# Kernel tuning notes

Measured on AMD Instinct MI355X. Metric: run time of the kernel, lower is better.

The kernel has to match this reference:

```python
import jax, jax.numpy as jnp
import numpy as np

N, C, D, E = 50000, 8, 64, 100000   # nodes, columns, dim, edges
L, H, FF, OUT = 2, 4, 64, 16        # layers, heads, dim_feedforward, out_channels
HD = D // H
EPS = 1e-5


def layer_norm(x, g, b):
    m = jnp.mean(x, axis=-1, keepdims=True)
    v = jnp.mean(jnp.square(x - m), axis=-1, keepdims=True)
    return (x - m) * jax.lax.rsqrt(v + EPS) * g + b


def encoder_layer(x, ipw, ipb, opw, opb, g1, b1, g2, b2, w1, bb1, w2, bb2):
    # x: [E, S, D]; post-norm TransformerEncoderLayer, relu, dropout=0 (eval)
    qkv = x @ ipw.T + ipb                      # [E, S, 3D]
    q, k, v = jnp.split(qkv, 3, axis=-1)
    Eb, S, _ = x.shape
    q = q.reshape(Eb, S, H, HD)
    k = k.reshape(Eb, S, H, HD)
    v = v.reshape(Eb, S, H, HD)
    scores = jnp.einsum('eqhd,ekhd->ehqk', q, k) / jnp.sqrt(jnp.asarray(HD, x.dtype))
    attn = jax.nn.softmax(scores, axis=-1)
    o = jnp.einsum('ehqk,ekhd->eqhd', attn, v).reshape(Eb, S, D)
    o = o @ opw.T + opb
    x = layer_norm(x + o, g1, b1)
    ff = jax.nn.relu(x @ w1.T + bb1) @ w2.T + bb2
    return layer_norm(x + ff, g2, b2)


def setup_inputs() -> dict:
    key = jax.random.key(0)
    ks = jax.random.split(key, 20)
    s = lambda *sh: 1.0 / np.sqrt(sh[-1])
    inp = {
        'x': jax.random.normal(ks[0], (N, C), jnp.float32),
        'edge_index': jax.random.randint(ks[1], (2, E), 0, N, jnp.int64),
        # NumEmbedder: per-column scalar -> D linear
        'num_w': jax.random.normal(ks[2], (C, D), jnp.float32) * 0.1,
        'num_b': jax.random.normal(ks[3], (C, D), jnp.float32) * 0.1,
        # per-layer TransformerGNN params (stacked over L)
        'bproj_w': jax.random.normal(ks[4], (L, D, D), jnp.float32) * s(D, D),
        'bproj_b': jnp.zeros((L, D), jnp.float32),
        'in_proj_w': jax.random.normal(ks[5], (L, 3 * D, D), jnp.float32) * s(D, D),
        'in_proj_b': jnp.zeros((L, 3 * D), jnp.float32),
        'out_proj_w': jax.random.normal(ks[6], (L, D, D), jnp.float32) * s(D, D),
        'out_proj_b': jnp.zeros((L, D), jnp.float32),
        'ln1_g': jnp.ones((L, D), jnp.float32), 'ln1_b': jnp.zeros((L, D), jnp.float32),
        'ln2_g': jnp.ones((L, D), jnp.float32), 'ln2_b': jnp.zeros((L, D), jnp.float32),
        'ff1_w': jax.random.normal(ks[7], (L, FF, D), jnp.float32) * s(FF, D),
        'ff1_b': jnp.zeros((L, FF), jnp.float32),
        'ff2_w': jax.random.normal(ks[8], (L, D, FF), jnp.float32) * s(D, FF),
        'ff2_b': jnp.zeros((L, D), jnp.float32),
        'out_w': jax.random.normal(ks[9], (OUT, D), jnp.float32) * s(OUT, D),
        'out_b': jnp.zeros((OUT,), jnp.float32),
    }
    return inp


def reference(x, edge_index, num_w, num_b, bproj_w, bproj_b, in_proj_w, in_proj_b,
              out_proj_w, out_proj_b, ln1_g, ln1_b, ln2_g, ln2_b,
              ff1_w, ff1_b, ff2_w, ff2_b, out_w, out_b):
    # column embedding: [N, C] -> [N, C, D] -> [N, C*D]
    h = (x[:, :, None] * num_w[None] + num_b[None]).reshape(N, C * D)
    src, tgt = edge_index[0], edge_index[1]
    cnt = jnp.clip(jax.ops.segment_sum(jnp.ones((E,), h.dtype), tgt, num_segments=N), 1.0)[:, None]
    for l in range(L):
        x_i = h[tgt].reshape(E, C, D)
        x_j = h[src].reshape(E, C, D) @ bproj_w[l].T + bproj_b[l]
        xc = jnp.concatenate([x_i, x_j], axis=1)              # [E, 2C, D]
        t = encoder_layer(xc, in_proj_w[l], in_proj_b[l], out_proj_w[l], out_proj_b[l],
                          ln1_g[l], ln1_b[l], ln2_g[l], ln2_b[l],
                          ff1_w[l], ff1_b[l], ff2_w[l], ff2_b[l])
        msg = t[:, :C, :].reshape(E, C * D)                   # slice target tokens
        h = jax.ops.segment_sum(msg, tgt, num_segments=N) / cnt  # mean aggr
    z = h.reshape(N, C, D) @ out_w.T + out_b                  # [N, C, OUT]
    z = jnp.sum(z, axis=1)
    return jax.nn.softmax(z, axis=1)
```

## Files before the change

### kernel.cpp

```cpp
#include <hip/hip_runtime.h>
#include <hip/hip_bf16.h>

#define NN 50000
#define EE 100000
#define LL 2

typedef __attribute__((ext_vector_type(8))) short short8;
typedef __attribute__((ext_vector_type(4))) float f32x4;

__device__ __forceinline__ short f2bf(float x) {
    __hip_bfloat16 b = __float2bfloat16(x);
    short s;
    __builtin_memcpy(&s, &b, 2);
    return s;
}
__device__ __forceinline__ unsigned us(short v) { return (unsigned)(unsigned short)v; }


__global__ __launch_bounds__(256)
void count_kernel(const int* __restrict__ tgt, int* __restrict__ cnt) {
    int e = blockIdx.x * 256 + threadIdx.x;
    if (e < EE) atomicAdd(&cnt[tgt[e]], 1);
}

__global__ __launch_bounds__(1024)
void scan_kernel(const int* __restrict__ cnt, int* __restrict__ off) {
    __shared__ int tmp[1024];
    __shared__ int carry;
    if (threadIdx.x == 0) carry = 0;
    __syncthreads();
    for (int base = 0; base < NN; base += 1024) {
        int i = base + threadIdx.x;
        int v = (i < NN) ? cnt[i] : 0;
        tmp[threadIdx.x] = v;
        __syncthreads();
        for (int d = 1; d < 1024; d <<= 1) {
            int t = (threadIdx.x >= d) ? tmp[threadIdx.x - d] : 0;
            __syncthreads();
            tmp[threadIdx.x] += t;
            __syncthreads();
        }
        int incl = tmp[threadIdx.x] + carry;
        if (i < NN) off[i + 1] = incl;
        __syncthreads();
        if (threadIdx.x == 1023) carry = incl;
        __syncthreads();
    }
    if (threadIdx.x == 0) off[0] = 0;
}

__global__ __launch_bounds__(256)
void fill_kernel(const int* __restrict__ tgt, const int* __restrict__ off,
                 int* __restrict__ fil, int* __restrict__ eidx) {
    int e = blockIdx.x * 256 + threadIdx.x;
    if (e < EE) {
        int t = tgt[e];
        int s = atomicAdd(&fil[t], 1);
        eidx[off[t] + s] = e;
    }
}

__global__ __launch_bounds__(256)
void recip_kernel(const int* __restrict__ cnt, float* __restrict__ rcnt) {
    int n = blockIdx.x * 256 + threadIdx.x;
    if (n < NN) rcnt[n] = 1.0f / fmaxf((float)cnt[n], 1.0f);
}

__global__ __launch_bounds__(256)
void embed_kernel(const float* __restrict__ x, const float* __restrict__ nw,
                  const float* __restrict__ nb, float* __restrict__ h0) {
    int gid = blockIdx.x * 256 + threadIdx.x;
    if (gid >= NN * 512) return;
    int n = gid >> 9, j = gid & 511;
    h0[gid] = x[n * 8 + (j >> 6)] * nw[j] + nb[j];
}

__global__ __launch_bounds__(256)
void prep_frags(const float* __restrict__ bpw, const float* __restrict__ ipw,
                const float* __restrict__ opw, const float* __restrict__ f1w,
                const float* __restrict__ f2w, short* __restrict__ wtb) {
    int gid = blockIdx.x * 256 + threadIdx.x;
    if (gid >= LL * 28672) return;
    int l = gid / 28672, u = gid % 28672;
    int f = u >> 9;
    int el = u & 511;
    int ln = el >> 3, j = el & 7;
    int row16 = ln & 15, kg = ln >> 4;
    const float* W;
    int t;
    if (f < 8)       { W = bpw + l * 4096;  t = f; }
    else if (f < 32) { W = ipw + l * 12288; t = f - 8; }
    else if (f < 40) { W = opw + l * 4096;  t = f - 32; }
    else if (f < 48) { W = f1w + l * 4096;  t = f - 40; }
    else             { W = f2w + l * 4096;  t = f - 48; }
    int nt = t >> 1, ks = t & 1;
    int r = nt * 16 + row16, col = ks * 32 + kg * 8 + j;
    wtb[(size_t)l * 28672 + u] = f2bf(W[r * 64 + col]);
}

__global__ __launch_bounds__(256)
void prep_fused(const float* __restrict__ bpw, const float* __restrict__ ipw,
                short* __restrict__ fwb) {
    int gid = blockIdx.x * 256 + threadIdx.x;
    if (gid >= LL * 8192) return;
    int l = gid / 8192, u2 = gid % 8192;
    int mat = u2 / 4096, u = u2 % 4096;
    int f = u >> 9, el = u & 511;
    int ln = el >> 3, j = el & 7;
    int row16 = ln & 15, kg = ln >> 4;
    int nt = f >> 1, ks = f & 1;
    int o = nt * 16 + row16, kcol = ks * 32 + kg * 8 + j;
    const float* Wx = ipw + l * 12288 + (64 + mat * 64 + o) * 64;
    const float* Wb = bpw + l * 4096;
    float s = 0.f;
#pragma unroll 8
    for (int m = 0; m < 64; m++) s = fmaf(Wx[m], Wb[m * 64 + kcol], s);
    fwb[gid] = f2bf(s);
}

__global__ __launch_bounds__(256)
void prep_fbias(const float* __restrict__ bpb, const float* __restrict__ ipw,
                const float* __restrict__ ipb, float* __restrict__ fbias) {
    int tid = blockIdx.x * 256 + threadIdx.x;
    if (tid >= LL * 128) return;
    int l = tid / 128, mo = tid % 128;
    int mat = mo / 64, o = mo % 64;
    const float* Wx = ipw + l * 12288 + (64 + mat * 64 + o) * 64;
    float s = ipb[l * 192 + 64 + mat * 64 + o];
#pragma unroll 8
    for (int m = 0; m < 64; m++) s = fmaf(Wx[m], bpb[l * 64 + m], s);
    fbias[tid] = s;
}


__device__ __forceinline__ void ln64(float x[4][4], const float* gv, const float* bv, int c) {
    float gg[4], bb[4];
#pragma unroll
    for (int nt = 0; nt < 4; nt++) { gg[nt] = gv[nt * 16 + c]; bb[nt] = bv[nt * 16 + c]; }
#pragma unroll
    for (int r = 0; r < 4; r++) {
        float s1 = x[0][r] + x[1][r] + x[2][r] + x[3][r];
        float s2 = x[0][r] * x[0][r];
#pragma unroll
        for (int nt = 1; nt < 4; nt++) s2 = fmaf(x[nt][r], x[nt][r], s2);
#pragma unroll
        for (int m = 1; m < 16; m <<= 1) { s1 += __shfl_xor(s1, m); s2 += __shfl_xor(s2, m); }
        float mean = s1 * 0.015625f;
        float var = fmaf(s2, 0.015625f, -mean * mean);
        float rs = rsqrtf(var + 1e-5f);
#pragma unroll
        for (int nt = 0; nt < 4; nt++) x[nt][r] = fmaf((x[nt][r] - mean) * rs, gg[nt], bb[nt]);
    }
}

__device__ __forceinline__ short8 cvt8(float4 lo, float4 hi) {
    short8 r;
    r[0] = f2bf(lo.x); r[1] = f2bf(lo.y); r[2] = f2bf(lo.z); r[3] = f2bf(lo.w);
    r[4] = f2bf(hi.x); r[5] = f2bf(hi.y); r[6] = f2bf(hi.z); r[7] = f2bf(hi.w);
    return r;
}

#define MFMA(a, b, cc) __builtin_amdgcn_mfma_f32_16x16x32_bf16((a), (b), (cc), 0, 0, 0)


__global__ __launch_bounds__(512, 2)
void layer_kernel(const float* __restrict__ h_in, short* __restrict__ msgp,
                  const int* __restrict__ src, const int* __restrict__ tgt,
                  const short* __restrict__ wfr, const short* __restrict__ fwb,
                  const float* __restrict__ fbl,
                  const float* __restrict__ ipb, const float* __restrict__ opb,
                  const float* __restrict__ g1v, const float* __restrict__ b1v,
                  const float* __restrict__ g2v, const float* __restrict__ b2v,
                  const float* __restrict__ f1b, const float* __restrict__ f2b)
{
    __shared__ __align__(16) char smem[158720];
    const int tid = threadIdx.x, wv = tid >> 6, lane = tid & 63;
    const int g = lane >> 4, c = lane & 15;
    const int swz = (c & 7) << 4;

    {
        int4* dw = (int4*)smem;
        const int4* s1 = (const int4*)(wfr + 8 * 512);
        for (int i = tid; i < 1536; i += 512) dw[i] = s1[i];
        const int4* s2 = (const int4*)fwb;
        for (int i = tid; i < 1024; i += 512) dw[1536 + i] = s2[i];
        const int4* s3 = (const int4*)(wfr + 32 * 512);
        for (int i = tid; i < 1024; i += 512) dw[2560 + i] = s3[i];
        float* bl = (float*)(smem + 57344);
        for (int i = tid; i < 768; i += 512) {
            float v;
            if (i < 192)      v = ipb[i];
            else if (i < 320) v = fbl[i - 192];
            else if (i < 384) v = opb[i - 320];
            else if (i < 448) v = g1v[i - 384];
            else if (i < 512) v = b1v[i - 448];
            else if (i < 576) v = g2v[i - 512];
            else if (i < 640) v = b2v[i - 576];
            else if (i < 704) v = f1b[i - 640];
            else              v = f2b[i - 704];
            bl[i] = v;
        }
    }
    __syncthreads();

    const short8* gw = (const short8*)wfr;
    short8 wf2[8];
#pragma unroll
    for (int i = 0; i < 8; i++) wf2[i] = gw[(48 + i) * 64 + lane];

    char* wb  = smem + 60416 + wv * 12288;
    char* tKA = wb;          char* tKB = wb + 2048;
    char* tQA = wb + 4096;   char* tQB = wb + 6144;
    char* VtA = wb + 8192;   char* VtB = wb + 10240;
    char* bufB = tQA;
    const float* bl = (const float*)(smem + 57344);
    const f32x4 zf = {};
    const short8 z8 = {};

    *(int4*)(tQA + 1024 + lane * 16) = make_int4(0, 0, 0, 0);
    *(int4*)(tQB + 1024 + lane * 16) = make_int4(0, 0, 0, 0);

#define LF(i)      (*(const short8*)&smem[(i) * 1024 + lane * 16])
#define LDA(B, ks) (*(const short8*)&(B)[c * 128 + (((ks) * 64 + g * 16) ^ swz)])
#define LDH(B, hh) (*(const short8*)&(B)[c * 128 + (((hh) * 32 + (g & 1) * 16) ^ swz)])

    const int P0 = blockIdx.x * 8 + wv;
    for (int p = P0; p < EE / 2; p += 2048) {
        const int eA = 2 * p, eB = 2 * p + 1;
        const int tnA = tgt[eA], snA = src[eA];
        const int tnB = tgt[eB], snB = src[eB];
        const float* hA  = h_in + (size_t)tnA * 512;
        const float* hB  = h_in + (size_t)tnB * 512;
        const float* hsA = h_in + (size_t)snA * 512;
        const float* hsB = h_in + (size_t)snB * 512;

        const float* hres = (g < 2) ? hA : hB;
        float xc[4][4];
#pragma unroll
        for (int nt = 0; nt < 4; nt++)
#pragma unroll
            for (int r = 0; r < 4; r++)
                xc[nt][r] = hres[((g & 1) * 4 + r) * 64 + nt * 16 + c];

        const float* rowA = (c < 8) ? (hA + c * 64) : (hB + (c - 8) * 64);
        const float* rowB = (c < 8) ? (hsA + c * 64) : (hsB + (c - 8) * 64);
        short8 a0 = cvt8(*(const float4*)(rowA + g * 8), *(const float4*)(rowA + g * 8 + 4));
        short8 a1 = cvt8(*(const float4*)(rowA + 32 + g * 8), *(const float4*)(rowA + 32 + g * 8 + 4));
        short8 b0 = cvt8(*(const float4*)(rowB + g * 8), *(const float4*)(rowB + g * 8 + 4));
        short8 b1f = cvt8(*(const float4*)(rowB + 32 + g * 8), *(const float4*)(rowB + 32 + g * 8 + 4));

        char* tK = (g < 2) ? tKA : tKB;
        char* tQ = (g < 2) ? tQA : tQB;
        char* Vt = (g < 2) ? VtA : VtB;
        const int lr4 = (g & 1) * 4;

#pragma unroll
        for (int nt = 0; nt < 4; nt++) {
            f32x4 qv = MFMA(a1, LF(nt * 2 + 1),      MFMA(a0, LF(nt * 2),      zf));
            f32x4 kv = MFMA(a1, LF(8 + nt * 2 + 1),  MFMA(a0, LF(8 + nt * 2),  zf));
            f32x4 vv = MFMA(a1, LF(16 + nt * 2 + 1), MFMA(a0, LF(16 + nt * 2), zf));
            float bq = bl[nt * 16 + c], bk = bl[64 + nt * 16 + c], bv = bl[128 + nt * 16 + c];
            int col2 = (nt * 16 + c) * 2;
#pragma unroll
            for (int r = 0; r < 4; r++) {
                int l2 = lr4 + r;
                int so = col2 ^ (l2 << 4);
                *(short*)(tK + l2 * 128 + so) = f2bf(kv[r] + bk);
                *(short*)(tQ + l2 * 128 + so) = f2bf(qv[r] + bq);
            }
            unsigned lo = us(f2bf(vv[0] + bv)) | (us(f2bf(vv[1] + bv)) << 16);
            unsigned hi = us(f2bf(vv[2] + bv)) | (us(f2bf(vv[3] + bv)) << 16);
            *(uint2*)(Vt + (nt * 16 + c) * 32 + (g & 1) * 8) = make_uint2(lo, hi);
        }

#pragma unroll
        for (int nt = 0; nt < 4; nt++) {
            f32x4 kj = MFMA(b1f, LF(24 + nt * 2 + 1), MFMA(b0, LF(24 + nt * 2), zf));
            f32x4 vj = MFMA(b1f, LF(32 + nt * 2 + 1), MFMA(b0, LF(32 + nt * 2), zf));
            float bk = bl[192 + nt * 16 + c], bv = bl[256 + nt * 16 + c];
            int col2 = (nt * 16 + c) * 2;
#pragma unroll
            for (int r = 0; r < 4; r++) {
                int l2 = lr4 + r;
                *(short*)(tK + (8 + l2) * 128 + (col2 ^ (l2 << 4))) = f2bf(kj[r] + bk);
            }
            unsigned lo = us(f2bf(vj[0] + bv)) | (us(f2bf(vj[1] + bv)) << 16);
            unsigned hi = us(f2bf(vj[2] + bv)) | (us(f2bf(vj[3] + bv)) << 16);
            *(uint2*)(Vt + (nt * 16 + c) * 32 + 16 + (g & 1) * 8) = make_uint2(lo, hi);
        }

        float ovA[4][4], ovB[4][4];
#pragma unroll
        for (int hh = 0; hh < 4; hh++) {
            short8 kfA = LDH(tKA, hh), qfA = LDH(tQA, hh);
            short8 kfB = LDH(tKB, hh), qfB = LDH(tQB, hh);
            if (lane >= 32) { kfA = z8; kfB = z8; }
            f32x4 stA = MFMA(kfA, qfA, zf);
            f32x4 stB = MFMA(kfB, qfB, zf);
            float pA[4], pB[4];
#pragma unroll
            for (int r = 0; r < 4; r++) { pA[r] = stA[r] * 0.25f; pB[r] = stB[r] * 0.25f; }
            float mA = fmaxf(fmaxf(pA[0], pA[1]), fmaxf(pA[2], pA[3]));
            float mB = fmaxf(fmaxf(pB[0], pB[1]), fmaxf(pB[2], pB[3]));
            mA = fmaxf(mA, __shfl_xor(mA, 16)); mB = fmaxf(mB, __shfl_xor(mB, 16));
            mA = fmaxf(mA, __shfl_xor(mA, 32)); mB = fmaxf(mB, __shfl_xor(mB, 32));
            float sA = 0.f, sB = 0.f;
#pragma unroll
            for (int r = 0; r < 4; r++) {
                pA[r] = __expf(pA[r] - mA); sA += pA[r];
                pB[r] = __expf(pB[r] - mB); sB += pB[r];
            }
            sA += __shfl_xor(sA, 16); sB += __shfl_xor(sB, 16);
            sA += __shfl_xor(sA, 32); sB += __shfl_xor(sB, 32);
            float iA = 1.0f / sA, iB = 1.0f / sB;
#pragma unroll
            for (int r = 0; r < 4; r++) { pA[r] *= iA; pB[r] *= iB; }

            short8 paA, paB;
#pragma unroll
            for (int j = 0; j < 8; j++) {
                int srcl = g * 32 + ((j >> 2) << 4) + c;
                paA[j] = f2bf(__shfl(pA[j & 3], srcl));
                paB[j] = f2bf(__shfl(pB[j & 3], srcl));
            }
            if (lane >= 32) { paA = z8; paB = z8; }
            short8 vbA = *(const short8*)&VtA[(hh * 16 + c) * 32 + (g & 1) * 16];
            short8 vbB = *(const short8*)&VtB[(hh * 16 + c) * 32 + (g & 1) * 16];
            f32x4 oA = MFMA(paA, vbA, zf);
            f32x4 oB = MFMA(paB, vbB, zf);
#pragma unroll
            for (int r = 0; r < 4; r++) { ovA[hh][r] = oA[r]; ovB[hh][r] = oB[r]; }
        }

        if (lane < 32) {
#pragma unroll
            for (int hh = 0; hh < 4; hh++)
#pragma unroll
                for (int r = 0; r < 4; r++) {
                    int m = g * 4 + r;
                    int so = ((hh * 16 + c) * 2) ^ (m << 4);
                    *(short*)&bufB[m * 128 + so] = f2bf(ovA[hh][r]);
                    *(short*)&bufB[(8 + m) * 128 + so] = f2bf(ovB[hh][r]);
                }
        }

        short8 c0 = LDA(bufB, 0), c1 = LDA(bufB, 1);
        float x1[4][4];
#pragma unroll
        for (int nt = 0; nt < 4; nt++) {
            f32x4 acc = MFMA(c1, LF(40 + nt * 2 + 1), MFMA(c0, LF(40 + nt * 2), zf));
            float bo = bl[320 + nt * 16 + c];
#pragma unroll
            for (int r = 0; r < 4; r++) x1[nt][r] = acc[r] + bo + xc[nt][r];
        }
        ln64(x1, bl + 384, bl + 448, c);

#pragma unroll
        for (int nt = 0; nt < 4; nt++)
#pragma unroll
            for (int r = 0; r < 4; r++) {
                int m = g * 4 + r;
                *(short*)&bufB[m * 128 + (((nt * 16 + c) * 2) ^ ((m & 7) << 4))] = f2bf(x1[nt][r]);
            }
        c0 = LDA(bufB, 0); c1 = LDA(bufB, 1);
#pragma unroll
        for (int nt = 0; nt < 4; nt++) {
            f32x4 acc = MFMA(c1, LF(48 + nt * 2 + 1), MFMA(c0, LF(48 + nt * 2), zf));
            float bf = bl[640 + nt * 16 + c];
#pragma unroll
            for (int r = 0; r < 4; r++) {
                float y = fmaxf(acc[r] + bf, 0.0f);
                int m = g * 4 + r;
                *(short*)&bufB[m * 128 + (((nt * 16 + c) * 2) ^ ((m & 7) << 4))] = f2bf(y);
            }
        }
        c0 = LDA(bufB, 0); c1 = LDA(bufB, 1);
        float x2[4][4];
#pragma unroll
        for (int nt = 0; nt < 4; nt++) {
            f32x4 acc = MFMA(c1, wf2[nt * 2 + 1], MFMA(c0, wf2[nt * 2], zf));
            float bf = bl[704 + nt * 16 + c];
#pragma unroll
            for (int r = 0; r < 4; r++) x2[nt][r] = acc[r] + bf + x1[nt][r];
        }
        ln64(x2, bl + 512, bl + 576, c);

        {
            unsigned w[8];
#pragma unroll
            for (int nt = 0; nt < 4; nt++) {
                unsigned a = us(f2bf(x2[nt][0]));
                unsigned b = us(f2bf(x2[nt][1]));
                unsigned cc2 = us(f2bf(x2[nt][2]));
                unsigned d = us(f2bf(x2[nt][3]));
                w[nt * 2]     = a | (b << 16);
                w[nt * 2 + 1] = cc2 | (d << 16);
            }
            int eOut = (lane < 32) ? eA : eB;
            int ll = lane & 31;
            char* me = (char*)(msgp + (size_t)eOut * 512) + ll * 32;
            ((int4*)me)[0] = make_int4(w[0], w[1], w[2], w[3]);
            ((int4*)me)[1] = make_int4(w[4], w[5], w[6], w[7]);
        }
    }
#undef LF
#undef LDA
#undef LDH
}


__global__ __launch_bounds__(256)
void aggr_kernel(const short* __restrict__ msgp, const int* __restrict__ off,
                 const int* __restrict__ eidx, const float* __restrict__ rcnt,
                 float* __restrict__ h) {
    int n = blockIdx.x * 4 + (threadIdx.x >> 6);
    if (n >= NN) return;
    int lane = threadIdx.x & 63;
    int b = off[n], t = off[n + 1];
    float acc[8] = {0, 0, 0, 0, 0, 0, 0, 0};
    for (int s = b; s < t; s++) {
        int e = eidx[s];
        short8 mv = *(const short8*)&msgp[(size_t)e * 512 + lane * 8];
#pragma unroll
        for (int j = 0; j < 8; j++)
            acc[j] += __uint_as_float(((unsigned)(unsigned short)mv[j]) << 16);
    }
    float rc = rcnt[n];
    float* hn = h + (size_t)n * 512;
#pragma unroll
    for (int j = 0; j < 8; j++) {
        int m = lane * 8 + j;
        int ls = m >> 4, u = m & 15;
        int hidx = ((ls >> 4) * 4 + (u & 3)) * 64 + (u >> 2) * 16 + (ls & 15);
        hn[hidx] = acc[j] * rc;
    }
}


__global__ __launch_bounds__(256)
void out_kernel(const float* __restrict__ h, const float* __restrict__ ow,
                const float* __restrict__ ob, float* __restrict__ out)
{
    __shared__ __align__(16) float hl[16 * 516];
    __shared__ __align__(16) float wl[16 * 68];
    __shared__ float blr[16];
    const int tid = threadIdx.x;
    const int n0 = blockIdx.x * 16;
#pragma unroll
    for (int i = 0; i < 4; i++) {
        int idx = i * 256 + tid;
        wl[(idx >> 6) * 68 + (idx & 63)] = ow[idx];
    }
    if (tid < 16) blr[tid] = ob[tid];
#pragma unroll
    for (int i = 0; i < 32; i++) {
        int idx = i * 256 + tid; int nl = idx >> 9, j = idx & 511;
        hl[nl * 516 + j] = h[(size_t)(n0 + nl) * 512 + j];
    }
    __syncthreads();
    const int nl = tid >> 4, o = tid & 15;
    float acc = 0;
#pragma unroll 4
    for (int d4 = 0; d4 < 16; d4++) {
        float4 wv = *(const float4*)&wl[o * 68 + d4 * 4];
#pragma unroll
        for (int cc = 0; cc < 8; cc++) {
            float4 hv = *(const float4*)&hl[nl * 516 + cc * 64 + d4 * 4];
            acc += hv.x * wv.x + hv.y * wv.y + hv.z * wv.z + hv.w * wv.w;
        }
    }
    float z = acc + 8.0f * blr[o];
    float mxv = z;
#pragma unroll
    for (int m = 1; m < 16; m <<= 1) mxv = fmaxf(mxv, __shfl_xor(mxv, m));
    float ez = __expf(z - mxv);
    float sm = ez;
#pragma unroll
    for (int m = 1; m < 16; m <<= 1) sm += __shfl_xor(sm, m);
    out[(size_t)(n0 + nl) * 16 + o] = ez / sm;
}


extern "C" void kernel_launch(void* const* d_in, const int* in_sizes, int n_in,
                              void* d_out, int out_size, void* d_ws, size_t ws_size,
                              hipStream_t stream)
{
    const float* x   = (const float*)d_in[0];
    const int*   ei  = (const int*)d_in[1];
    const float* nw  = (const float*)d_in[2];
    const float* nb  = (const float*)d_in[3];
    const float* bpw = (const float*)d_in[4];
    const float* bpb = (const float*)d_in[5];
    const float* ipw = (const float*)d_in[6];
    const float* ipb = (const float*)d_in[7];
    const float* opw = (const float*)d_in[8];
    const float* opb = (const float*)d_in[9];
    const float* g1  = (const float*)d_in[10];
    const float* b1  = (const float*)d_in[11];
    const float* g2  = (const float*)d_in[12];
    const float* b2  = (const float*)d_in[13];
    const float* f1w = (const float*)d_in[14];
    const float* f1b = (const float*)d_in[15];
    const float* f2w = (const float*)d_in[16];
    const float* f2b = (const float*)d_in[17];
    const float* ow  = (const float*)d_in[18];
    const float* ob  = (const float*)d_in[19];

    float* h0    = (float*)d_ws;
    short* msg   = (short*)(h0 + (size_t)NN * 512);
    int*   cnt   = (int*)(msg + (size_t)EE * 512);
    int*   off   = cnt + 50000;
    int*   fil   = off + 50004;
    int*   eidx  = fil + 50000;
    float* rcnt  = (float*)(eidx + 100000);
    short* wtb   = (short*)(rcnt + 50000);
    short* fwb   = wtb + LL * 28672;
    float* fbias = (float*)(fwb + LL * 8192);

    hipMemsetAsync(cnt, 0, 50000 * sizeof(int), stream);
    hipMemsetAsync(fil, 0, 50000 * sizeof(int), stream);
    count_kernel<<<(EE + 255) / 256, 256, 0, stream>>>(ei + EE, cnt);
    scan_kernel<<<1, 1024, 0, stream>>>(cnt, off);
    fill_kernel<<<(EE + 255) / 256, 256, 0, stream>>>(ei + EE, off, fil, eidx);
    recip_kernel<<<(NN + 255) / 256, 256, 0, stream>>>(cnt, rcnt);
    prep_frags<<<(LL * 28672 + 255) / 256, 256, 0, stream>>>(bpw, ipw, opw, f1w, f2w, wtb);
    prep_fused<<<(LL * 8192 + 255) / 256, 256, 0, stream>>>(bpw, ipw, fwb);
    prep_fbias<<<1, 256, 0, stream>>>(bpb, ipw, ipb, fbias);
    embed_kernel<<<(NN * 512) / 256, 256, 0, stream>>>(x, nw, nb, h0);

    for (int l = 0; l < LL; l++) {
        layer_kernel<<<256, 512, 0, stream>>>(
            h0, msg, ei, ei + EE, wtb + l * 28672, fwb + l * 8192, fbias + l * 128,
            ipb + l * 192, opb + l * 64, g1 + l * 64, b1 + l * 64,
            g2 + l * 64, b2 + l * 64, f1b + l * 64, f2b + l * 64);
        aggr_kernel<<<(NN + 3) / 4, 256, 0, stream>>>(msg, off, eidx, rcnt, h0);
    }
    out_kernel<<<NN / 16, 256, 0, stream>>>(h0, ow, ob, (float*)d_out);
}
```

Before: 787.8 us.

## Write messages in CSR order, prefetch next edge rows, fuse final aggregation into output

The fill pass now records each edge's slot in target-sorted order, and layer_kernel writes messages straight to that slot. Aggregation can then stream contiguous message rows instead of gathering through an edge index. The layer loop software-prefetches the next edge pair's indices and h rows into registers so global latency overlaps the current pair's MFMA work. The last aggr pass and its h write/read are folded into out_kernel, which sums messages on the fly and scatters them into the expected layout. The cost is higher register pressure from the prefetch buffers and extra index math in the output kernel.

```diff
diff --git a/kernel.cpp b/kernel.cpp
--- a/kernel.cpp
+++ b/kernel.cpp
@@ -51,12 +51,12 @@
 
 __global__ __launch_bounds__(256)
 void fill_kernel(const int* __restrict__ tgt, const int* __restrict__ off,
-                 int* __restrict__ fil, int* __restrict__ eidx) {
+                 int* __restrict__ fil, int* __restrict__ einv) {
     int e = blockIdx.x * 256 + threadIdx.x;
     if (e < EE) {
         int t = tgt[e];
         int s = atomicAdd(&fil[t], 1);
-        eidx[off[t] + s] = e;
+        einv[e] = off[t] + s;
     }
 }
 
@@ -166,6 +166,7 @@
 __global__ __launch_bounds__(512, 2)
 void layer_kernel(const float* __restrict__ h_in, short* __restrict__ msgp,
                   const int* __restrict__ src, const int* __restrict__ tgt,
+                  const int* __restrict__ einv,
                   const short* __restrict__ wfr, const short* __restrict__ fwb,
                   const float* __restrict__ fbl,
                   const float* __restrict__ ipb, const float* __restrict__ opb,
@@ -186,7 +187,7 @@
         for (int i = tid; i < 1024; i += 512) dw[1536 + i] = s2[i];
         const int4* s3 = (const int4*)(wfr + 32 * 512);
         for (int i = tid; i < 1024; i += 512) dw[2560 + i] = s3[i];
-        float* bl = (float*)(smem + 57344);
+        float* bls = (float*)(smem + 57344);
         for (int i = tid; i < 768; i += 512) {
             float v;
             if (i < 192)      v = ipb[i];
@@ -198,7 +199,7 @@
             else if (i < 640) v = b2v[i - 576];
             else if (i < 704) v = f1b[i - 640];
             else              v = f2b[i - 704];
-            bl[i] = v;
+            bls[i] = v;
         }
     }
     __syncthreads();
@@ -225,29 +226,39 @@
 #define LDH(B, hh) (*(const short8*)&(B)[c * 128 + (((hh) * 32 + (g & 1) * 16) ^ swz)])
 
     const int P0 = blockIdx.x * 8 + wv;
-    for (int p = P0; p < EE / 2; p += 2048) {
-        const int eA = 2 * p, eB = 2 * p + 1;
-        const int tnA = tgt[eA], snA = src[eA];
-        const int tnB = tgt[eB], snB = src[eB];
+
+    int tnA = tgt[2 * P0], snA = src[2 * P0];
+    int tnB = tgt[2 * P0 + 1], snB = src[2 * P0 + 1];
+    int slA = einv[2 * P0], slB = einv[2 * P0 + 1];
+    float4 ra0, ra1, ra2, ra3, rb0, rb1, rb2, rb3;
+    float xcp[4][4];
+    {
         const float* hA  = h_in + (size_t)tnA * 512;
         const float* hB  = h_in + (size_t)tnB * 512;
-        const float* hsA = h_in + (size_t)snA * 512;
-        const float* hsB = h_in + (size_t)snB * 512;
-
+        const float* rowA = (c < 8) ? (hA + c * 64) : (hB + (c - 8) * 64);
+        const float* rowB = (c < 8) ? (h_in + (size_t)snA * 512 + c * 64)
+                                    : (h_in + (size_t)snB * 512 + (c - 8) * 64);
+        ra0 = *(const float4*)(rowA + g * 8);      ra1 = *(const float4*)(rowA + g * 8 + 4);
+        ra2 = *(const float4*)(rowA + 32 + g * 8); ra3 = *(const float4*)(rowA + 32 + g * 8 + 4);
+        rb0 = *(const float4*)(rowB + g * 8);      rb1 = *(const float4*)(rowB + g * 8 + 4);
+        rb2 = *(const float4*)(rowB + 32 + g * 8); rb3 = *(const float4*)(rowB + 32 + g * 8 + 4);
         const float* hres = (g < 2) ? hA : hB;
+#pragma unroll
+        for (int nt = 0; nt < 4; nt++)
+#pragma unroll
+            for (int r = 0; r < 4; r++)
+                xcp[nt][r] = hres[((g & 1) * 4 + r) * 64 + nt * 16 + c];
+    }
+
+    for (int p = P0; p < EE / 2; p += 2048) {
+        short8 a0 = cvt8(ra0, ra1), a1 = cvt8(ra2, ra3);
+        short8 b0 = cvt8(rb0, rb1), b1f = cvt8(rb2, rb3);
+        const int slotA = slA, slotB = slB;
         float xc[4][4];
 #pragma unroll
         for (int nt = 0; nt < 4; nt++)
 #pragma unroll
-            for (int r = 0; r < 4; r++)
-                xc[nt][r] = hres[((g & 1) * 4 + r) * 64 + nt * 16 + c];
-
-        const float* rowA = (c < 8) ? (hA + c * 64) : (hB + (c - 8) * 64);
-        const float* rowB = (c < 8) ? (hsA + c * 64) : (hsB + (c - 8) * 64);
-        short8 a0 = cvt8(*(const float4*)(rowA + g * 8), *(const float4*)(rowA + g * 8 + 4));
-        short8 a1 = cvt8(*(const float4*)(rowA + 32 + g * 8), *(const float4*)(rowA + 32 + g * 8 + 4));
-        short8 b0 = cvt8(*(const float4*)(rowB + g * 8), *(const float4*)(rowB + g * 8 + 4));
-        short8 b1f = cvt8(*(const float4*)(rowB + 32 + g * 8), *(const float4*)(rowB + 32 + g * 8 + 4));
+            for (int r = 0; r < 4; r++) xc[nt][r] = xcp[nt][r];
 
         char* tK = (g < 2) ? tKA : tKB;
         char* tQ = (g < 2) ? tQA : tQB;
@@ -287,6 +298,28 @@
             unsigned lo = us(f2bf(vj[0] + bv)) | (us(f2bf(vj[1] + bv)) << 16);
             unsigned hi = us(f2bf(vj[2] + bv)) | (us(f2bf(vj[3] + bv)) << 16);
             *(uint2*)(Vt + (nt * 16 + c) * 32 + 16 + (g & 1) * 8) = make_uint2(lo, hi);
+        }
+
+        {
+            int pn = p + 2048; if (2 * pn >= EE) pn = p;
+            tnA = tgt[2 * pn];     snA = src[2 * pn];
+            tnB = tgt[2 * pn + 1]; snB = src[2 * pn + 1];
+            slA = einv[2 * pn];    slB = einv[2 * pn + 1];
+            const float* hA  = h_in + (size_t)tnA * 512;
+            const float* hB  = h_in + (size_t)tnB * 512;
+            const float* rowA = (c < 8) ? (hA + c * 64) : (hB + (c - 8) * 64);
+            const float* rowB = (c < 8) ? (h_in + (size_t)snA * 512 + c * 64)
+                                        : (h_in + (size_t)snB * 512 + (c - 8) * 64);
+            ra0 = *(const float4*)(rowA + g * 8);      ra1 = *(const float4*)(rowA + g * 8 + 4);
+            ra2 = *(const float4*)(rowA + 32 + g * 8); ra3 = *(const float4*)(rowA + 32 + g * 8 + 4);
+            rb0 = *(const float4*)(rowB + g * 8);      rb1 = *(const float4*)(rowB + g * 8 + 4);
+            rb2 = *(const float4*)(rowB + 32 + g * 8); rb3 = *(const float4*)(rowB + 32 + g * 8 + 4);
+            const float* hres = (g < 2) ? hA : hB;
+#pragma unroll
+            for (int nt = 0; nt < 4; nt++)
+#pragma unroll
+                for (int r = 0; r < 4; r++)
+                    xcp[nt][r] = hres[((g & 1) * 4 + r) * 64 + nt * 16 + c];
         }
 
         float ovA[4][4], ovB[4][4];
@@ -396,9 +429,9 @@
                 w[nt * 2]     = a | (b << 16);
                 w[nt * 2 + 1] = cc2 | (d << 16);
             }
-            int eOut = (lane < 32) ? eA : eB;
+            int sOut = (lane < 32) ? slotA : slotB;
             int ll = lane & 31;
-            char* me = (char*)(msgp + (size_t)eOut * 512) + ll * 32;
+            char* me = (char*)(msgp + (size_t)sOut * 512) + ll * 32;
             ((int4*)me)[0] = make_int4(w[0], w[1], w[2], w[3]);
             ((int4*)me)[1] = make_int4(w[4], w[5], w[6], w[7]);
         }
@@ -411,16 +444,14 @@
 
 __global__ __launch_bounds__(256)
 void aggr_kernel(const short* __restrict__ msgp, const int* __restrict__ off,
-                 const int* __restrict__ eidx, const float* __restrict__ rcnt,
-                 float* __restrict__ h) {
+                 const float* __restrict__ rcnt, float* __restrict__ h) {
     int n = blockIdx.x * 4 + (threadIdx.x >> 6);
     if (n >= NN) return;
     int lane = threadIdx.x & 63;
     int b = off[n], t = off[n + 1];
     float acc[8] = {0, 0, 0, 0, 0, 0, 0, 0};
     for (int s = b; s < t; s++) {
-        int e = eidx[s];
-        short8 mv = *(const short8*)&msgp[(size_t)e * 512 + lane * 8];
+        short8 mv = *(const short8*)&msgp[(size_t)s * 512 + lane * 8];
 #pragma unroll
         for (int j = 0; j < 8; j++)
             acc[j] += __uint_as_float(((unsigned)(unsigned short)mv[j]) << 16);
@@ -438,13 +469,15 @@
 
 
 __global__ __launch_bounds__(256)
-void out_kernel(const float* __restrict__ h, const float* __restrict__ ow,
-                const float* __restrict__ ob, float* __restrict__ out)
+void out_kernel(const short* __restrict__ msgp, const int* __restrict__ off,
+                const float* __restrict__ rcnt,
+                const float* __restrict__ ow, const float* __restrict__ ob,
+                float* __restrict__ out)
 {
     __shared__ __align__(16) float hl[16 * 516];
     __shared__ __align__(16) float wl[16 * 68];
     __shared__ float blr[16];
-    const int tid = threadIdx.x;
+    const int tid = threadIdx.x, wv = tid >> 6, lane = tid & 63;
     const int n0 = blockIdx.x * 16;
 #pragma unroll
     for (int i = 0; i < 4; i++) {
@@ -452,21 +485,39 @@
         wl[(idx >> 6) * 68 + (idx & 63)] = ow[idx];
     }
     if (tid < 16) blr[tid] = ob[tid];
-#pragma unroll
-    for (int i = 0; i < 32; i++) {
-        int idx = i * 256 + tid; int nl = idx >> 9, j = idx & 511;
-        hl[nl * 516 + j] = h[(size_t)(n0 + nl) * 512 + j];
+
+#pragma unroll
+    for (int q = 0; q < 4; q++) {
+        int nl = wv * 4 + q;
+        int n = n0 + nl;
+        int b = off[n], t = off[n + 1];
+        float acc[8] = {0, 0, 0, 0, 0, 0, 0, 0};
+        for (int s = b; s < t; s++) {
+            short8 mv = *(const short8*)&msgp[(size_t)s * 512 + lane * 8];
+#pragma unroll
+            for (int j = 0; j < 8; j++)
+                acc[j] += __uint_as_float(((unsigned)(unsigned short)mv[j]) << 16);
+        }
+        float rc = rcnt[n];
+#pragma unroll
+        for (int j = 0; j < 8; j++) {
+            int m = lane * 8 + j;
+            int ls = m >> 4, u = m & 15;
+            int hidx = ((ls >> 4) * 4 + (u & 3)) * 64 + (u >> 2) * 16 + (ls & 15);
+            hl[nl * 516 + hidx] = acc[j] * rc;
+        }
     }
     __syncthreads();
+
     const int nl = tid >> 4, o = tid & 15;
     float acc = 0;
 #pragma unroll 4
     for (int d4 = 0; d4 < 16; d4++) {
-        float4 wv = *(const float4*)&wl[o * 68 + d4 * 4];
+        float4 wv4 = *(const float4*)&wl[o * 68 + d4 * 4];
 #pragma unroll
         for (int cc = 0; cc < 8; cc++) {
             float4 hv = *(const float4*)&hl[nl * 516 + cc * 64 + d4 * 4];
-            acc += hv.x * wv.x + hv.y * wv.y + hv.z * wv.z + hv.w * wv.w;
+            acc += hv.x * wv4.x + hv.y * wv4.y + hv.z * wv4.z + hv.w * wv4.w;
         }
     }
     float z = acc + 8.0f * blr[o];
@@ -511,8 +562,8 @@
     int*   cnt   = (int*)(msg + (size_t)EE * 512);
     int*   off   = cnt + 50000;
     int*   fil   = off + 50004;
-    int*   eidx  = fil + 50000;
-    float* rcnt  = (float*)(eidx + 100000);
+    int*   einv  = fil + 50000;
+    float* rcnt  = (float*)(einv + 100000);
     short* wtb   = (short*)(rcnt + 50000);
     short* fwb   = wtb + LL * 28672;
     float* fbias = (float*)(fwb + LL * 8192);
@@ -521,19 +572,19 @@
     hipMemsetAsync(fil, 0, 50000 * sizeof(int), stream);
     count_kernel<<<(EE + 255) / 256, 256, 0, stream>>>(ei + EE, cnt);
     scan_kernel<<<1, 1024, 0, stream>>>(cnt, off);
-    fill_kernel<<<(EE + 255) / 256, 256, 0, stream>>>(ei + EE, off, fil, eidx);
+    fill_kernel<<<(EE + 255) / 256, 256, 0, stream>>>(ei + EE, off, fil, einv);
     recip_kernel<<<(NN + 255) / 256, 256, 0, stream>>>(cnt, rcnt);
     prep_frags<<<(LL * 28672 + 255) / 256, 256, 0, stream>>>(bpw, ipw, opw, f1w, f2w, wtb);
     prep_fused<<<(LL * 8192 + 255) / 256, 256, 0, stream>>>(bpw, ipw, fwb);
     prep_fbias<<<1, 256, 0, stream>>>(bpb, ipw, ipb, fbias);
     embed_kernel<<<(NN * 512) / 256, 256, 0, stream>>>(x, nw, nb, h0);
 
-    for (int l = 0; l < LL; l++) {
-        layer_kernel<<<256, 512, 0, stream>>>(
-            h0, msg, ei, ei + EE, wtb + l * 28672, fwb + l * 8192, fbias + l * 128,
-            ipb + l * 192, opb + l * 64, g1 + l * 64, b1 + l * 64,
-            g2 + l * 64, b2 + l * 64, f1b + l * 64, f2b + l * 64);
-        aggr_kernel<<<(NN + 3) / 4, 256, 0, stream>>>(msg, off, eidx, rcnt, h0);
-    }
-    out_kernel<<<NN / 16, 256, 0, stream>>>(h0, ow, ob, (float*)d_out);
-}
+    layer_kernel<<<256, 512, 0, stream>>>(
+        h0, msg, ei, ei + EE, einv, wtb, fwb, fbias,
+        ipb, opb, g1, b1, g2, b2, f1b, f2b);
+    aggr_kernel<<<(NN + 3) / 4, 256, 0, stream>>>(msg, off, rcnt, h0);
+    layer_kernel<<<256, 512, 0, stream>>>(
+        h0, msg, ei, ei + EE, einv, wtb + 28672, fwb + 8192, fbias + 128,
+        ipb + 192, opb + 64, g1 + 64, b1 + 64, g2 + 64, b2 + 64, f1b + 64, f2b + 64);
+    out_kernel<<<NN / 16, 256, 0, stream>>>(msg, off, rcnt, ow, ob, (float*)d_out);
+}
```

Measured after the change: 788.4 us. No clear change (+0.1%).
